# Performance work log

Hardware: AMD Instinct MI355X
Metric: run time of the kernel (lower is better)

## Reference

```python
import jax, jax.numpy as jnp
import numpy as np

D_MODEL = 1024
N_HEADS = 16
D_FF = 4 * D_MODEL
EPS = 1e-5


def _layer_norm(x, g, b):
    mu = jnp.mean(x, axis=-1, keepdims=True)
    var = jnp.mean(jnp.square(x - mu), axis=-1, keepdims=True)
    return (x - mu) * jax.lax.rsqrt(var + EPS) * g + b


def _mha(x, Wq, Wk, Wv, Wo, causal):
    B, S, D = x.shape
    H = N_HEADS
    Dh = D // H
    q = (x @ Wq).reshape(B, S, H, Dh)
    k = (x @ Wk).reshape(B, S, H, Dh)
    v = (x @ Wv).reshape(B, S, H, Dh)
    scores = jnp.einsum('bqhd,bkhd->bhqk', q, k) / jnp.sqrt(jnp.asarray(Dh, x.dtype))
    if causal:
        mask = jnp.tril(jnp.ones((S, S), dtype=bool))  # [S,S] causal mask
        scores = jnp.where(mask, scores, jnp.asarray(-1e9, x.dtype))
    attn = jax.nn.softmax(scores, axis=-1)
    out = jnp.einsum('bhqk,bkhd->bqhd', attn, v).reshape(B, S, D)
    return out @ Wo


def _ffn(x, W1, b1, W2, b2):
    return jax.nn.relu(x @ W1 + b1) @ W2 + b2


def setup_inputs() -> dict:
    key = jax.random.key(0)
    ks = jax.random.split(key, 12)
    sd = 1.0 / np.sqrt(D_MODEL)
    sf = 1.0 / np.sqrt(D_FF)
    B, S = 4, 1024
    return {
        'X': jax.random.normal(ks[0], (B, S, D_MODEL), jnp.float32),
        'Wq1': jax.random.normal(ks[1], (D_MODEL, D_MODEL), jnp.float32) * sd,
        'Wk1': jax.random.normal(ks[2], (D_MODEL, D_MODEL), jnp.float32) * sd,
        'Wv1': jax.random.normal(ks[3], (D_MODEL, D_MODEL), jnp.float32) * sd,
        'Wo1': jax.random.normal(ks[4], (D_MODEL, D_MODEL), jnp.float32) * sd,
        'Wq2': jax.random.normal(ks[5], (D_MODEL, D_MODEL), jnp.float32) * sd,
        'Wk2': jax.random.normal(ks[6], (D_MODEL, D_MODEL), jnp.float32) * sd,
        'Wv2': jax.random.normal(ks[7], (D_MODEL, D_MODEL), jnp.float32) * sd,
        'Wo2': jax.random.normal(ks[8], (D_MODEL, D_MODEL), jnp.float32) * sd,
        'ln_g': jnp.ones((D_MODEL,), jnp.float32),
        'ln_b': jnp.zeros((D_MODEL,), jnp.float32),
        'W1': jax.random.normal(ks[9], (D_MODEL, D_FF), jnp.float32) * sd,
        'b1': jnp.zeros((D_FF,), jnp.float32),
        'W2': jax.random.normal(ks[10], (D_FF, D_MODEL), jnp.float32) * sf,
        'b2': jnp.zeros((D_MODEL,), jnp.float32),
    }


def reference(X, Wq1, Wk1, Wv1, Wo1, Wq2, Wk2, Wv2, Wo2, ln_g, ln_b, W1, b1, W2, b2):
    # Faithful to the torch module (including its unusual residual wiring
    # and the single shared LayerNorm used at all three sites).
    masked = _mha(X, Wq1, Wk1, Wv1, Wo1, causal=True)
    norm_masked = X + _layer_norm(masked, ln_g, ln_b)
    attn2 = _mha(norm_masked, Wq2, Wk2, Wv2, Wo2, causal=False)
    norm_attn2 = attn2 + _layer_norm(attn2, ln_g, ln_b)
    ff = _ffn(norm_attn2, W1, b1, W2, b2)
    return norm_attn2 + _layer_norm(ff, ln_g, ln_b)
```

## Files before the change

kernel.cpp:

```cpp
#include <hip/hip_runtime.h>
#include <hip/hip_bf16.h>

#define D_MODEL 1024
#define N_HEADS 16
#define DH 64
#define D_FF   4096
#define SEQ    1024
#define BATCH  4
#define TOK    (BATCH*SEQ)
#define EPS    1e-5f
#define SCALE  0.125f
#define QSCL   0.18033688f

typedef unsigned short USHORT;
typedef __attribute__((ext_vector_type(8))) short short8v;
typedef __attribute__((ext_vector_type(4))) float f32x4;

__device__ __forceinline__ USHORT f2bf(float f) {
    unsigned int u; __builtin_memcpy(&u, &f, 4);
    u += 0x7fffu + ((u >> 16) & 1u);
    return (USHORT)(u >> 16);
}
__device__ __forceinline__ USHORT f2bf_fast(float f) {
    unsigned int u; __builtin_memcpy(&u, &f, 4);
    return (USHORT)((u + 0x8000u) >> 16);
}
__device__ __forceinline__ unsigned pk2bf(float lo, float hi) {
    __hip_bfloat162 h = __float22bfloat162_rn(make_float2(lo, hi));
    unsigned u; __builtin_memcpy(&u, &h, 4);
    return u;
}
__device__ __forceinline__ float bf2f(USHORT s) {
    unsigned int u = ((unsigned int)s) << 16;
    float f; __builtin_memcpy(&f, &u, 4);
    return f;
}
__device__ __forceinline__ float max3f(float a, float b, float c) {
    return fmaxf(fmaxf(a, b), c);
}

__device__ __forceinline__ short8v ld_frag(const USHORT* lds, int row, int c8) {
    return *reinterpret_cast<const short8v*>(
        &lds[row * 64 + (((c8) ^ (row & 7)) << 3)]);
}
__device__ __forceinline__ short8v ld128(const USHORT* lds, int row, int cu) {
    return *reinterpret_cast<const short8v*>(
        &lds[row * 128 + (((cu) ^ (row & 15)) << 3)]);
}

#define GLDS(gsrc, ldst) \
    __builtin_amdgcn_global_load_lds( \
        (const __attribute__((address_space(1))) void*)(gsrc), \
        (__attribute__((address_space(3))) void*)(ldst), 16, 0, 0)

#define WAITVM(n) asm volatile("s_waitcnt vmcnt(" #n ")" ::: "memory")

__global__ __launch_bounds__(512) void gemm_k256_kernel(
    const USHORT* __restrict__ A, const USHORT* __restrict__ Bt,
    float* __restrict__ Cf, USHORT* __restrict__ Cb, USHORT* __restrict__ Ck,
    USHORT* __restrict__ VtOut,
    int M, int N, int K, const float* __restrict__ bias, int relu, int qkv)
{
    __shared__ USHORT As[2][256 * 64];
    __shared__ USHORT Bs[2][256 * 64];

    const int tid = threadIdx.x;
    const int l   = tid & 63;
    const int w   = tid >> 6;
    const int wr  = w >> 2, wc = w & 3;
    const int lr  = l & 15, lg = l >> 4;

    const int gx  = gridDim.x;
    const int nwg = gx * gridDim.y;
    const int lin = blockIdx.y * gx + blockIdx.x;
    const int swz = (lin & 7) * (nwg >> 3) + (lin >> 3);
    const int m0  = (swz / gx) * 256, n0 = (swz % gx) * 256;

    const USHORT* aS[4]; const USHORT* bS[4]; int dOf[4];
#pragma unroll
    for (int p = 0; p < 4; ++p) {
        const int q = p * 512 + tid;
        const int row = q >> 3, cu = q & 7;
        const int cs = ((cu ^ (row & 7)) << 3);
        aS[p] = A  + (size_t)(m0 + row) * K + cs;
        bS[p] = Bt + (size_t)(n0 + row) * K + cs;
        dOf[p] = (p * 512 + w * 64) * 8;
    }

    auto stage = [&](int buf, int k0) {
#pragma unroll
        for (int p = 0; p < 4; ++p) {
            GLDS(aS[p] + k0, &As[buf][dOf[p]]);
            GLDS(bS[p] + k0, &Bs[buf][dOf[p]]);
        }
    };

    f32x4 acc[8][4];
#pragma unroll
    for (int i = 0; i < 8; ++i)
#pragma unroll
        for (int j = 0; j < 4; ++j) acc[i][j] = (f32x4){0.f, 0.f, 0.f, 0.f};

    const int nk = K >> 6;
    stage(0, 0);

    for (int t = 0; t < nk; ++t) {
        const int cur = t & 1;
        if (t + 1 < nk) {
            stage(cur ^ 1, (t + 1) << 6);
            WAITVM(8);
        } else {
            WAITVM(0);
        }
        __builtin_amdgcn_s_barrier();

#pragma unroll
        for (int ks = 0; ks < 2; ++ks) {
            short8v bfr[4];
#pragma unroll
            for (int ni = 0; ni < 4; ++ni)
                bfr[ni] = ld_frag(Bs[cur], wc * 64 + ni * 16 + lr, ks * 4 + lg);
            __builtin_amdgcn_s_setprio(1);
#pragma unroll
            for (int mi = 0; mi < 8; ++mi) {
                short8v af = ld_frag(As[cur], wr * 128 + mi * 16 + lr, ks * 4 + lg);
#pragma unroll
                for (int ni = 0; ni < 4; ++ni)
                    acc[mi][ni] = __builtin_amdgcn_mfma_f32_16x16x32_bf16(
                        af, bfr[ni], acc[mi][ni], 0, 0, 0);
            }
            __builtin_amdgcn_s_setprio(0);
        }
        __builtin_amdgcn_s_barrier();
    }

    if (qkv) {
#pragma unroll
        for (int mi = 0; mi < 8; ++mi) {
            const int row = m0 + wr * 128 + mi * 16 + (l >> 4) * 4;
#pragma unroll
            for (int ni = 0; ni < 4; ++ni) {
                const int col = n0 + wc * 64 + ni * 16 + lr;
                if (col < 2048) {
                    USHORT* dst = (col < 1024) ? Cb : Ck;
                    const float scl = (col < 1024) ? QSCL : 1.f;
                    const int c = col & 1023;
#pragma unroll
                    for (int j = 0; j < 4; ++j)
                        dst[(size_t)(row + j) * D_MODEL + c] =
                            f2bf(acc[mi][ni][j] * scl);
                } else {
                    const int c = col - 2048;
                    const int bb = row >> 10, jr = row & 1023;
                    const int hh = c >> 6, dd = c & 63;
                    uint2 pk = make_uint2(
                        pk2bf(acc[mi][ni][0], acc[mi][ni][1]),
                        pk2bf(acc[mi][ni][2], acc[mi][ni][3]));
                    *reinterpret_cast<uint2*>(
                        &VtOut[((size_t)(bb * 16 + hh) * 64 + dd) * 1024 + jr]) = pk;
                }
            }
        }
    } else {
#pragma unroll
        for (int mi = 0; mi < 8; ++mi) {
            const int row = m0 + wr * 128 + mi * 16 + (l >> 4) * 4;
#pragma unroll
            for (int ni = 0; ni < 4; ++ni) {
                const int col = n0 + wc * 64 + ni * 16 + lr;
                const float bv = bias ? bias[col] : 0.f;
#pragma unroll
                for (int j = 0; j < 4; ++j) {
                    float v = acc[mi][ni][j] + bv;
                    if (relu) v = fmaxf(v, 0.f);
                    const size_t idx = (size_t)(row + j) * N + col;
                    if (Cf) Cf[idx] = v;
                    if (Cb) Cb[idx] = f2bf(v);
                }
            }
        }
    }
}

__global__ __launch_bounds__(512) void gemm_k128c_kernel(
    const USHORT* __restrict__ A, const USHORT* __restrict__ Bt,
    USHORT* __restrict__ Pa, USHORT* __restrict__ Pb,
    int M, int N, int K)
{
    __shared__ USHORT As[2][128 * 64];
    __shared__ USHORT Bs[2][128 * 64];

    const int tid = threadIdx.x;
    const int l   = tid & 63;
    const int w   = tid >> 6;
    const int wr  = w >> 2, wc = w & 3;
    const int lr  = l & 15, lg = l >> 4;

    const int gx  = gridDim.x;
    const int nwg = gx * gridDim.y;
    const int lin = blockIdx.y * gx + blockIdx.x;
    const int swz = (lin & 7) * (nwg >> 3) + (lin >> 3);
    const int my  = swz / gx;
    const int mt  = M >> 7;
    const int part = my / mt;
    const int m0  = (my % mt) << 7;
    const int n0  = (swz % gx) * 128;
    const int koff = part * (K >> 1);
    USHORT* dst = part ? Pb : Pa;

    const USHORT* aS[2]; const USHORT* bS[2]; int dOf[2];
#pragma unroll
    for (int p = 0; p < 2; ++p) {
        const int q = p * 512 + tid;
        const int row = q >> 3, cu = q & 7;
        const int cs = ((cu ^ (row & 7)) << 3);
        aS[p] = A  + (size_t)(m0 + row) * K + cs;
        bS[p] = Bt + (size_t)(n0 + row) * K + cs;
        dOf[p] = (p * 512 + w * 64) * 8;
    }

    auto stage = [&](int buf, int k0) {
#pragma unroll
        for (int p = 0; p < 2; ++p) {
            GLDS(aS[p] + k0, &As[buf][dOf[p]]);
            GLDS(bS[p] + k0, &Bs[buf][dOf[p]]);
        }
    };

    f32x4 acc[4][2];
#pragma unroll
    for (int i = 0; i < 4; ++i)
#pragma unroll
        for (int j = 0; j < 2; ++j) acc[i][j] = (f32x4){0.f, 0.f, 0.f, 0.f};

    const int nk = K >> 7;
    stage(0, koff);

    for (int t = 0; t < nk; ++t) {
        const int cur = t & 1;
        if (t + 1 < nk) {
            stage(cur ^ 1, koff + ((t + 1) << 6));
            WAITVM(4);
        } else {
            WAITVM(0);
        }
        __builtin_amdgcn_s_barrier();

#pragma unroll
        for (int ks = 0; ks < 2; ++ks) {
            short8v bfr[2];
#pragma unroll
            for (int ni = 0; ni < 2; ++ni)
                bfr[ni] = ld_frag(Bs[cur], wc * 32 + ni * 16 + lr, ks * 4 + lg);
            __builtin_amdgcn_s_setprio(1);
#pragma unroll
            for (int mi = 0; mi < 4; ++mi) {
                short8v af = ld_frag(As[cur], wr * 64 + mi * 16 + lr, ks * 4 + lg);
#pragma unroll
                for (int ni = 0; ni < 2; ++ni)
                    acc[mi][ni] = __builtin_amdgcn_mfma_f32_16x16x32_bf16(
                        af, bfr[ni], acc[mi][ni], 0, 0, 0);
            }
            __builtin_amdgcn_s_setprio(0);
        }
        __builtin_amdgcn_s_barrier();
    }

#pragma unroll
    for (int mi = 0; mi < 4; ++mi) {
        const int row = m0 + wr * 64 + mi * 16 + (l >> 4) * 4;
#pragma unroll
        for (int ni = 0; ni < 2; ++ni) {
            const int col = n0 + wc * 32 + ni * 16 + lr;
#pragma unroll
            for (int j = 0; j < 4; ++j)
                dst[(size_t)(row + j) * N + col] = f2bf(acc[mi][ni][j]);
        }
    }
}

struct TcvtB4 {
    const float* s0; const float* s1; const float* s2; const float* s3;
    USHORT* d0; USHORT* d1; USHORT* d2; USHORT* d3;
};

__device__ __forceinline__ void tcvt_body(
    const float* __restrict__ W, USHORT* __restrict__ Wt, int K, int N)
{
    __shared__ USHORT L[64][65];
    const int tid = threadIdx.x;
    const int tx = tid & 15, ty = tid >> 4;
    const int n0 = blockIdx.x * 64, k0 = blockIdx.y * 64;
#pragma unroll
    for (int r = 0; r < 4; ++r) {
        int kr = ty + 16 * r;
        float4 v = *reinterpret_cast<const float4*>(
            &W[(size_t)(k0 + kr) * N + n0 + tx * 4]);
        L[tx * 4 + 0][kr] = f2bf(v.x);
        L[tx * 4 + 1][kr] = f2bf(v.y);
        L[tx * 4 + 2][kr] = f2bf(v.z);
        L[tx * 4 + 3][kr] = f2bf(v.w);
    }
    __syncthreads();
#pragma unroll
    for (int r = 0; r < 4; ++r) {
        int nr = ty + 16 * r;
        ushort4 o = make_ushort4(L[nr][tx * 4 + 0], L[nr][tx * 4 + 1],
                                 L[nr][tx * 4 + 2], L[nr][tx * 4 + 3]);
        *reinterpret_cast<ushort4*>(&Wt[(size_t)(n0 + nr) * K + k0 + tx * 4]) = o;
    }
}

__global__ __launch_bounds__(256) void tcvt_kernel(
    const float* __restrict__ W, USHORT* __restrict__ Wt, int K, int N)
{
    tcvt_body(W, Wt, K, N);
}

__global__ __launch_bounds__(256) void tcvt4_kernel(TcvtB4 p, int K, int N)
{
    const int z = blockIdx.z;
    const float* W = (z == 0) ? p.s0 : (z == 1) ? p.s1 : (z == 2) ? p.s2 : p.s3;
    USHORT*    Wt = (z == 0) ? p.d0 : (z == 1) ? p.d1 : (z == 2) ? p.d2 : p.d3;
    tcvt_body(W, Wt, K, N);
}

__global__ __launch_bounds__(256) void f2b_kernel(
    const float* __restrict__ in, USHORT* __restrict__ out, int n4)
{
    int i = blockIdx.x * 256 + threadIdx.x;
    if (i < n4) {
        float4 v = reinterpret_cast<const float4*>(in)[i];
        reinterpret_cast<ushort4*>(out)[i] =
            make_ushort4(f2bf(v.x), f2bf(v.y), f2bf(v.z), f2bf(v.w));
    }
}

__global__ __launch_bounds__(256) void attn_mfma_kernel(
    const USHORT* __restrict__ Q, const USHORT* __restrict__ K,
    const USHORT* __restrict__ Vt, USHORT* __restrict__ O, int causal)
{
    __shared__ USHORT smem[40960];

    const int tid = threadIdx.x;
    const int l  = tid & 63;
    const int w  = tid >> 6;
    const int lr = l & 15;
    const int lg = l >> 4;

    const int lin = blockIdx.y * 16 + blockIdx.x;
    const int swz = (lin & 7) * 128 + (lin >> 3);
    const int qt = swz & 15;
    const int bh = swz >> 4;
    const int h = bh & 15, b = bh >> 4;
    const int q0 = qt * 64;

    const USHORT* gq  = Q  + (size_t)(b * SEQ + q0) * D_MODEL + h * DH;
    const USHORT* gk0 = K  + (size_t)b * SEQ * D_MODEL + h * DH;
    const USHORT* gv0 = Vt + (size_t)bh * DH * SEQ;

    auto stageK = [&](int buf, int kt) {
        USHORT* dst = smem + buf * 8192;
        const size_t base = (size_t)kt * 128 * 1024;
#pragma unroll
        for (int p = 0; p < 4; ++p) {
            const int q = p * 256 + tid;
            const int row = q >> 3, cu = q & 7;
            GLDS(gk0 + base + (size_t)row * 1024 + ((cu ^ (row & 7)) << 3),
                 dst + (p * 256 + w * 64) * 8);
        }
    };
    auto stageV = [&](int buf, int kt) {
        USHORT* dst = smem + 16384 + buf * 8192;
        const int j0 = kt * 128;
#pragma unroll
        for (int p = 0; p < 4; ++p) {
            const int q = p * 256 + tid;
            const int row = q >> 4, cu = q & 15;
            GLDS(gv0 + (size_t)row * 1024 + j0 + ((cu ^ (row & 15)) << 3),
                 dst + (p * 256 + w * 64) * 8);
        }
    };

#pragma unroll
    for (int p = 0; p < 2; ++p) {
        const int q = p * 256 + tid;
        const int row = q >> 3, cu = q & 7;
        GLDS(gq + (size_t)row * 1024 + ((cu ^ (row & 7)) << 3),
             smem + 32768 + (p * 256 + w * 64) * 8);
    }
    stageK(0, 0);
    stageV(0, 0);

    f32x4 oacc[4];
    float m_ = -1e30f, l_ = 0.f;
#pragma unroll
    for (int d = 0; d < 4; ++d) oacc[d] = (f32x4){0.f, 0.f, 0.f, 0.f};

    int paddr[8];
#pragma unroll
    for (int jb = 0; jb < 8; ++jb) {
        const int cu = jb * 2 + (lg >> 1);
        paddr[jb] = lr * 128 + ((cu ^ lr) << 3) + (lg & 1) * 4;
    }

    __syncthreads();
    short8v qa0 = ld_frag(smem + 32768, w * 16 + lr, lg);
    short8v qa1 = ld_frag(smem + 32768, w * 16 + lr, 4 + lg);
    __syncthreads();
    USHORT* PsW = smem + 32768 + w * 2048;

    const int ntile = causal ? (qt >> 1) + 1 : (SEQ / 128);
    for (int kt = 0; kt < ntile; ++kt) {
        const int cur = kt & 1;
        if (kt + 1 < ntile) {
            stageK(cur ^ 1, kt + 1);
            stageV(cur ^ 1, kt + 1);
        }
        const int j0 = kt * 128;
        const USHORT* KsC = smem + cur * 8192;
        const USHORT* VsC = smem + 16384 + cur * 8192;

        f32x4 sa[8];
        __builtin_amdgcn_s_setprio(1);
#pragma unroll
        for (int jb = 0; jb < 8; ++jb) {
            sa[jb] = (f32x4){0.f, 0.f, 0.f, 0.f};
            sa[jb] = __builtin_amdgcn_mfma_f32_16x16x32_bf16(
                ld_frag(KsC, jb * 16 + lr, lg), qa0, sa[jb], 0, 0, 0);
            sa[jb] = __builtin_amdgcn_mfma_f32_16x16x32_bf16(
                ld_frag(KsC, jb * 16 + lr, 4 + lg), qa1, sa[jb], 0, 0, 0);
        }
        __builtin_amdgcn_s_setprio(0);

        if (causal && kt == ntile - 1) {
#pragma unroll
            for (int jb = 0; jb < 8; ++jb)
#pragma unroll
                for (int r = 0; r < 4; ++r)
                    if ((j0 + jb * 16 + lg * 4 + r) > (q0 + w * 16 + lr))
                        sa[jb][r] = -1e30f;
        }

        float tm = max3f(
            max3f(max3f(sa[0][0], sa[0][1], sa[0][2]),
                  max3f(sa[0][3], sa[1][0], sa[1][1]),
                  max3f(sa[1][2], sa[1][3], sa[2][0])),
            max3f(max3f(sa[2][1], sa[2][2], sa[2][3]),
                  max3f(sa[3][0], sa[3][1], sa[3][2]),
                  max3f(sa[3][3], sa[4][0], sa[4][1])),
            max3f(max3f(max3f(sa[4][2], sa[4][3], sa[5][0]),
                        max3f(sa[5][1], sa[5][2], sa[5][3]),
                        max3f(sa[6][0], sa[6][1], sa[6][2])),
                  max3f(sa[6][3], sa[7][0], sa[7][1]),
                  fmaxf(sa[7][2], sa[7][3])));
        tm = fmaxf(tm, __shfl_xor(tm, 16));
        tm = fmaxf(tm, __shfl_xor(tm, 32));

        if (__ballot(tm > m_ + 8.f)) {
            const float mn = (tm > m_ + 8.f) ? tm : m_;
            const float sc = exp2f(m_ - mn);
            l_ *= sc;
            m_ = mn;
#pragma unroll
            for (int r = 0; r < 4; ++r) {
                const float scr = __shfl(sc, (l & 48) | (lg * 4 + r));
#pragma unroll
                for (int d = 0; d < 4; ++d) oacc[d][r] *= scr;
            }
        }

#pragma unroll
        for (int jb = 0; jb < 8; ++jb) {
            const float p0 = exp2f(sa[jb][0] - m_);
            const float p1 = exp2f(sa[jb][1] - m_);
            const float p2 = exp2f(sa[jb][2] - m_);
            const float p3 = exp2f(sa[jb][3] - m_);
            l_ += (p0 + p1) + (p2 + p3);
            *reinterpret_cast<uint2*>(&PsW[paddr[jb]]) =
                make_uint2(pk2bf(p0, p1), pk2bf(p2, p3));
        }

        __builtin_amdgcn_s_setprio(1);
#pragma unroll
        for (int ks = 0; ks < 4; ++ks) {
            short8v pa = ld128(PsW, lr, ks * 4 + lg);
#pragma unroll
            for (int d = 0; d < 4; ++d)
                oacc[d] = __builtin_amdgcn_mfma_f32_16x16x32_bf16(
                    pa, ld128(VsC, d * 16 + lr, ks * 4 + lg), oacc[d], 0, 0, 0);
        }
        __builtin_amdgcn_s_setprio(0);
        __syncthreads();
    }

    float lv = l_;
    lv += __shfl_xor(lv, 16);
    lv += __shfl_xor(lv, 32);
    const float inv_own = 1.f / lv;

    USHORT* go = O + (size_t)(b * SEQ + q0 + w * 16) * D_MODEL + h * DH;
#pragma unroll
    for (int r = 0; r < 4; ++r) {
        const float inv = __shfl(inv_own, (l & 48) | (lg * 4 + r));
        const int qrow = lg * 4 + r;
#pragma unroll
        for (int d = 0; d < 4; ++d)
            go[(size_t)qrow * D_MODEL + d * 16 + lr] = f2bf_fast(oacc[d][r] * inv);
    }
}

__global__ __launch_bounds__(256) void ln_res_kernel(
    const USHORT* __restrict__ xb, const USHORT* __restrict__ xb2,
    const float* __restrict__ biasx,
    const float* __restrict__ resf, const USHORT* __restrict__ resb,
    const float* __restrict__ g, const float* __restrict__ bta,
    float* __restrict__ outf, USHORT* __restrict__ outb)
{
    __shared__ float red[256];
    __shared__ float s_mu, s_rstd;

    const int row = blockIdx.x;
    const int tid = threadIdx.x;
    ushort4 xv = reinterpret_cast<const ushort4*>(xb + (size_t)row * D_MODEL)[tid];
    float vx = bf2f(xv.x), vy = bf2f(xv.y), vz = bf2f(xv.z), vw = bf2f(xv.w);
    if (xb2) {
        ushort4 x2 = reinterpret_cast<const ushort4*>(
            xb2 + (size_t)row * D_MODEL)[tid];
        vx += bf2f(x2.x); vy += bf2f(x2.y); vz += bf2f(x2.z); vw += bf2f(x2.w);
    }
    if (biasx) {
        float4 bx = reinterpret_cast<const float4*>(biasx)[tid];
        vx += bx.x; vy += bx.y; vz += bx.z; vw += bx.w;
    }

    red[tid] = vx + vy + vz + vw;
    __syncthreads();
    for (int s = 128; s > 0; s >>= 1) {
        if (tid < s) red[tid] += red[tid + s];
        __syncthreads();
    }
    if (tid == 0) s_mu = red[0] * (1.f / D_MODEL);
    __syncthreads();
    const float mu = s_mu;

    float dx = vx - mu, dy = vy - mu, dz = vz - mu, dw = vw - mu;
    red[tid] = dx * dx + dy * dy + dz * dz + dw * dw;
    __syncthreads();
    for (int s = 128; s > 0; s >>= 1) {
        if (tid < s) red[tid] += red[tid + s];
        __syncthreads();
    }
    if (tid == 0) s_rstd = rsqrtf(red[0] * (1.f / D_MODEL) + EPS);
    __syncthreads();
    const float rstd = s_rstd;

    float4 rv;
    if (resf) {
        rv = reinterpret_cast<const float4*>(resf + (size_t)row * D_MODEL)[tid];
    } else if (resb) {
        ushort4 rb = reinterpret_cast<const ushort4*>(
            resb + (size_t)row * D_MODEL)[tid];
        rv = make_float4(bf2f(rb.x), bf2f(rb.y), bf2f(rb.z), bf2f(rb.w));
    } else {
        rv = make_float4(vx, vy, vz, vw);
    }
    float4 gv = reinterpret_cast<const float4*>(g)[tid];
    float4 bv = reinterpret_cast<const float4*>(bta)[tid];

    float4 o;
    o.x = rv.x + dx * rstd * gv.x + bv.x;
    o.y = rv.y + dy * rstd * gv.y + bv.y;
    o.z = rv.z + dz * rstd * gv.z + bv.z;
    o.w = rv.w + dw * rstd * gv.w + bv.w;
    reinterpret_cast<float4*>(outf + (size_t)row * D_MODEL)[tid] = o;
    if (outb)
        reinterpret_cast<ushort4*>(outb + (size_t)row * D_MODEL)[tid] =
            make_ushort4(f2bf(o.x), f2bf(o.y), f2bf(o.z), f2bf(o.w));
}

extern "C" void kernel_launch(void* const* d_in, const int* in_sizes, int n_in,
                              void* d_out, int out_size, void* d_ws, size_t ws_size,
                              hipStream_t stream)
{
    const float* X    = (const float*)d_in[0];
    const float* Wq1  = (const float*)d_in[1];
    const float* Wk1  = (const float*)d_in[2];
    const float* Wv1  = (const float*)d_in[3];
    const float* Wo1  = (const float*)d_in[4];
    const float* Wq2  = (const float*)d_in[5];
    const float* Wk2  = (const float*)d_in[6];
    const float* Wv2  = (const float*)d_in[7];
    const float* Wo2  = (const float*)d_in[8];
    const float* ln_g = (const float*)d_in[9];
    const float* ln_b = (const float*)d_in[10];
    const float* W1   = (const float*)d_in[11];
    const float* b1   = (const float*)d_in[12];
    const float* W2   = (const float*)d_in[13];
    const float* b2   = (const float*)d_in[14];

    const size_t MI = 1024 * 1024;
    USHORT* ws16 = (USHORT*)d_ws;
    USHORT* Wqkv1t = ws16;
    USHORT* scr0   = ws16;
    USHORT* Wo1t   = ws16 + 3 * MI;
    USHORT* Wqkv2t = ws16 + 4 * MI;
    USHORT* Wo2t   = ws16 + 7 * MI;
    USHORT* W2t    = ws16 + 8 * MI;
    USHORT* Xb     = ws16 + 12 * MI;
    USHORT* W1t    = Xb;
    USHORT* qb     = ws16 + 16 * MI;
    USHORT* kb     = ws16 + 20 * MI;
    USHORT* Vtb    = ws16 + 24 * MI;
    USHORT* t0b    = ws16 + 28 * MI;
    USHORT* hb     = qb;
    USHORT* t2b    = ws16 + 32 * MI;
    USHORT* t1b    = ws16 + 36 * MI;
    float*  t2     = (float*)(ws16 + 40 * MI);

    auto gemm256 = [&](const USHORT* A, const USHORT* Bt, float* Cf, USHORT* Cb,
                       int M, int N, int K, const float* bias, int relu) {
        gemm_k256_kernel<<<dim3(N / 256, M / 256), 512, 0, stream>>>(
            A, Bt, Cf, Cb, nullptr, nullptr, M, N, K, bias, relu, 0);
    };
    auto gemm_qkv = [&](const USHORT* A, const USHORT* Bt) {
        gemm_k256_kernel<<<dim3(3072 / 256, TOK / 256), 512, 0, stream>>>(
            A, Bt, nullptr, qb, kb, Vtb, TOK, 3072, D_MODEL, nullptr, 0, 1);
    };
    auto gemm128c = [&](const USHORT* A, const USHORT* Bt, USHORT* Pa, USHORT* Pb,
                        int M, int N, int K) {
        gemm_k128c_kernel<<<dim3(N / 128, (M / 128) * 2), 512, 0, stream>>>(
            A, Bt, Pa, Pb, M, N, K);
    };

    dim3 agrid(SEQ / 64, BATCH * N_HEADS);

    {
        TcvtB4 p1{Wq1, Wk1, Wv1, Wo1,
                  Wqkv1t, Wqkv1t + 1 * MI, Wqkv1t + 2 * MI, Wo1t};
        tcvt4_kernel<<<dim3(16, 16, 4), 256, 0, stream>>>(p1, D_MODEL, D_MODEL);
        TcvtB4 p2{Wq2, Wk2, Wv2, Wo2,
                  Wqkv2t, Wqkv2t + 1 * MI, Wqkv2t + 2 * MI, Wo2t};
        tcvt4_kernel<<<dim3(16, 16, 4), 256, 0, stream>>>(p2, D_MODEL, D_MODEL);
    }
    tcvt_kernel<<<dim3(D_MODEL / 64, D_FF / 64), 256, 0, stream>>>(
        W2, W2t, D_FF, D_MODEL);
    f2b_kernel<<<dim3(4096), 256, 0, stream>>>(X, Xb, TOK * D_MODEL / 4);

    gemm_qkv(Xb, Wqkv1t);
    attn_mfma_kernel<<<agrid, 256, 0, stream>>>(qb, kb, Vtb, t0b, 1);
    gemm128c(t0b, Wo1t, t2b, t1b, TOK, D_MODEL, D_MODEL);
    ln_res_kernel<<<dim3(TOK), 256, 0, stream>>>(t2b, t1b, nullptr, X, nullptr,
                                                 ln_g, ln_b, t2, t2b);
    tcvt_kernel<<<dim3(D_FF / 64, D_MODEL / 64), 256, 0, stream>>>(
        W1, W1t, D_MODEL, D_FF);

    gemm_qkv(t2b, Wqkv2t);
    attn_mfma_kernel<<<agrid, 256, 0, stream>>>(qb, kb, Vtb, t0b, 0);
    gemm128c(t0b, Wo2t, scr0, t1b, TOK, D_MODEL, D_MODEL);
    ln_res_kernel<<<dim3(TOK), 256, 0, stream>>>(scr0, t1b, nullptr,
                                                 nullptr, nullptr,
                                                 ln_g, ln_b, t2, t2b);

    gemm256(t2b, W1t, nullptr, hb, TOK, D_FF, D_MODEL, b1, 1);
    gemm128c(hb, W2t, t2b, t1b, TOK, D_MODEL, D_FF);
    ln_res_kernel<<<dim3(TOK), 256, 0, stream>>>(t2b, t1b, b2, t2, nullptr,
                                                 ln_g, ln_b, (float*)d_out, nullptr);
}
```

Measured before the change: 338.3 us.

## Retile attention to 128-query blocks with 64-key tiles, two subtiles per wave

The attention kernel now processes 128 query rows per block, with each wave owning two 16-row subtiles, and streams K/V in 64-key tiles instead of 128. Each K and V fragment loaded from LDS is reused across two MFMA subtiles, and shared memory per block shrinks. The intent is to halve K/V global and LDS traffic per query and improve MFMA density. In exchange the grid is halved, which may reduce occupancy and load balance (especially for causal), and more registers are used per thread.

```diff
diff --git a/kernel.cpp b/kernel.cpp
--- a/kernel.cpp
+++ b/kernel.cpp
@@ -42,10 +42,6 @@
 __device__ __forceinline__ short8v ld_frag(const USHORT* lds, int row, int c8) {
     return *reinterpret_cast<const short8v*>(
         &lds[row * 64 + (((c8) ^ (row & 7)) << 3)]);
-}
-__device__ __forceinline__ short8v ld128(const USHORT* lds, int row, int cu) {
-    return *reinterpret_cast<const short8v*>(
-        &lds[row * 128 + (((cu) ^ (row & 15)) << 3)]);
 }
 
 #define GLDS(gsrc, ldst) \
@@ -340,7 +336,7 @@
     const USHORT* __restrict__ Q, const USHORT* __restrict__ K,
     const USHORT* __restrict__ Vt, USHORT* __restrict__ O, int causal)
 {
-    __shared__ USHORT smem[40960];
+    __shared__ USHORT smem[24576];
 
     const int tid = threadIdx.x;
     const int l  = tid & 63;
@@ -348,22 +344,22 @@
     const int lr = l & 15;
     const int lg = l >> 4;
 
-    const int lin = blockIdx.y * 16 + blockIdx.x;
-    const int swz = (lin & 7) * 128 + (lin >> 3);
-    const int qt = swz & 15;
-    const int bh = swz >> 4;
+    const int lin = blockIdx.y * 8 + blockIdx.x;
+    const int swz = (lin & 7) * 64 + (lin >> 3);
+    const int qt = swz & 7;
+    const int bh = swz >> 3;
     const int h = bh & 15, b = bh >> 4;
-    const int q0 = qt * 64;
+    const int q0 = qt * 128;
 
     const USHORT* gq  = Q  + (size_t)(b * SEQ + q0) * D_MODEL + h * DH;
     const USHORT* gk0 = K  + (size_t)b * SEQ * D_MODEL + h * DH;
     const USHORT* gv0 = Vt + (size_t)bh * DH * SEQ;
 
     auto stageK = [&](int buf, int kt) {
-        USHORT* dst = smem + buf * 8192;
-        const size_t base = (size_t)kt * 128 * 1024;
-#pragma unroll
-        for (int p = 0; p < 4; ++p) {
+        USHORT* dst = smem + buf * 4096;
+        const size_t base = (size_t)kt * 64 * 1024;
+#pragma unroll
+        for (int p = 0; p < 2; ++p) {
             const int q = p * 256 + tid;
             const int row = q >> 3, cu = q & 7;
             GLDS(gk0 + base + (size_t)row * 1024 + ((cu ^ (row & 7)) << 3),
@@ -371,142 +367,181 @@
         }
     };
     auto stageV = [&](int buf, int kt) {
-        USHORT* dst = smem + 16384 + buf * 8192;
-        const int j0 = kt * 128;
-#pragma unroll
-        for (int p = 0; p < 4; ++p) {
+        USHORT* dst = smem + 8192 + buf * 4096;
+        const int j0 = kt * 64;
+#pragma unroll
+        for (int p = 0; p < 2; ++p) {
             const int q = p * 256 + tid;
-            const int row = q >> 4, cu = q & 15;
-            GLDS(gv0 + (size_t)row * 1024 + j0 + ((cu ^ (row & 15)) << 3),
+            const int row = q >> 3, cu = q & 7;
+            GLDS(gv0 + (size_t)row * 1024 + j0 + ((cu ^ (row & 7)) << 3),
                  dst + (p * 256 + w * 64) * 8);
         }
     };
 
 #pragma unroll
-    for (int p = 0; p < 2; ++p) {
+    for (int p = 0; p < 4; ++p) {
         const int q = p * 256 + tid;
         const int row = q >> 3, cu = q & 7;
         GLDS(gq + (size_t)row * 1024 + ((cu ^ (row & 7)) << 3),
-             smem + 32768 + (p * 256 + w * 64) * 8);
+             smem + 16384 + (p * 256 + w * 64) * 8);
     }
     stageK(0, 0);
     stageV(0, 0);
 
-    f32x4 oacc[4];
-    float m_ = -1e30f, l_ = 0.f;
-#pragma unroll
-    for (int d = 0; d < 4; ++d) oacc[d] = (f32x4){0.f, 0.f, 0.f, 0.f};
-
-    int paddr[8];
-#pragma unroll
-    for (int jb = 0; jb < 8; ++jb) {
-        const int cu = jb * 2 + (lg >> 1);
-        paddr[jb] = lr * 128 + ((cu ^ lr) << 3) + (lg & 1) * 4;
+    f32x4 oacc[2][4];
+    float m_[2], l_[2];
+#pragma unroll
+    for (int s = 0; s < 2; ++s) {
+        m_[s] = -1e30f; l_[s] = 0.f;
+#pragma unroll
+        for (int d = 0; d < 4; ++d) oacc[s][d] = (f32x4){0.f, 0.f, 0.f, 0.f};
+    }
+
+    int paddr[2][4];
+#pragma unroll
+    for (int s = 0; s < 2; ++s) {
+        const int row = s * 16 + lr;
+#pragma unroll
+        for (int jb = 0; jb < 4; ++jb) {
+            const int cu = jb * 2 + (lg >> 1);
+            paddr[s][jb] = row * 64 + ((cu ^ (row & 7)) << 3) + (lg & 1) * 4;
+        }
     }
 
     __syncthreads();
-    short8v qa0 = ld_frag(smem + 32768, w * 16 + lr, lg);
-    short8v qa1 = ld_frag(smem + 32768, w * 16 + lr, 4 + lg);
+    short8v qa[2][2];
+#pragma unroll
+    for (int s = 0; s < 2; ++s) {
+        qa[s][0] = ld_frag(smem + 16384, w * 32 + s * 16 + lr, lg);
+        qa[s][1] = ld_frag(smem + 16384, w * 32 + s * 16 + lr, 4 + lg);
+    }
     __syncthreads();
-    USHORT* PsW = smem + 32768 + w * 2048;
-
-    const int ntile = causal ? (qt >> 1) + 1 : (SEQ / 128);
+    USHORT* PsW = smem + 16384 + w * 2048;
+
+    const int ntile = causal ? (qt * 2 + 2) : (SEQ / 64);
     for (int kt = 0; kt < ntile; ++kt) {
         const int cur = kt & 1;
         if (kt + 1 < ntile) {
             stageK(cur ^ 1, kt + 1);
             stageV(cur ^ 1, kt + 1);
         }
-        const int j0 = kt * 128;
-        const USHORT* KsC = smem + cur * 8192;
-        const USHORT* VsC = smem + 16384 + cur * 8192;
-
-        f32x4 sa[8];
+        const int j0 = kt * 64;
+        const USHORT* KsC = smem + cur * 4096;
+        const USHORT* VsC = smem + 8192 + cur * 4096;
+
+        f32x4 sa[2][4];
         __builtin_amdgcn_s_setprio(1);
 #pragma unroll
-        for (int jb = 0; jb < 8; ++jb) {
-            sa[jb] = (f32x4){0.f, 0.f, 0.f, 0.f};
-            sa[jb] = __builtin_amdgcn_mfma_f32_16x16x32_bf16(
-                ld_frag(KsC, jb * 16 + lr, lg), qa0, sa[jb], 0, 0, 0);
-            sa[jb] = __builtin_amdgcn_mfma_f32_16x16x32_bf16(
-                ld_frag(KsC, jb * 16 + lr, 4 + lg), qa1, sa[jb], 0, 0, 0);
+        for (int jb = 0; jb < 4; ++jb) {
+            short8v kf0 = ld_frag(KsC, jb * 16 + lr, lg);
+            short8v kf1 = ld_frag(KsC, jb * 16 + lr, 4 + lg);
+#pragma unroll
+            for (int s = 0; s < 2; ++s) {
+                sa[s][jb] = (f32x4){0.f, 0.f, 0.f, 0.f};
+                sa[s][jb] = __builtin_amdgcn_mfma_f32_16x16x32_bf16(
+                    kf0, qa[s][0], sa[s][jb], 0, 0, 0);
+                sa[s][jb] = __builtin_amdgcn_mfma_f32_16x16x32_bf16(
+                    kf1, qa[s][1], sa[s][jb], 0, 0, 0);
+            }
         }
         __builtin_amdgcn_s_setprio(0);
 
-        if (causal && kt == ntile - 1) {
-#pragma unroll
-            for (int jb = 0; jb < 8; ++jb)
-#pragma unroll
-                for (int r = 0; r < 4; ++r)
-                    if ((j0 + jb * 16 + lg * 4 + r) > (q0 + w * 16 + lr))
-                        sa[jb][r] = -1e30f;
-        }
-
-        float tm = max3f(
-            max3f(max3f(sa[0][0], sa[0][1], sa[0][2]),
-                  max3f(sa[0][3], sa[1][0], sa[1][1]),
-                  max3f(sa[1][2], sa[1][3], sa[2][0])),
-            max3f(max3f(sa[2][1], sa[2][2], sa[2][3]),
-                  max3f(sa[3][0], sa[3][1], sa[3][2]),
-                  max3f(sa[3][3], sa[4][0], sa[4][1])),
-            max3f(max3f(max3f(sa[4][2], sa[4][3], sa[5][0]),
-                        max3f(sa[5][1], sa[5][2], sa[5][3]),
-                        max3f(sa[6][0], sa[6][1], sa[6][2])),
-                  max3f(sa[6][3], sa[7][0], sa[7][1]),
-                  fmaxf(sa[7][2], sa[7][3])));
-        tm = fmaxf(tm, __shfl_xor(tm, 16));
-        tm = fmaxf(tm, __shfl_xor(tm, 32));
-
-        if (__ballot(tm > m_ + 8.f)) {
-            const float mn = (tm > m_ + 8.f) ? tm : m_;
-            const float sc = exp2f(m_ - mn);
-            l_ *= sc;
-            m_ = mn;
-#pragma unroll
-            for (int r = 0; r < 4; ++r) {
-                const float scr = __shfl(sc, (l & 48) | (lg * 4 + r));
-#pragma unroll
-                for (int d = 0; d < 4; ++d) oacc[d][r] *= scr;
-            }
-        }
-
-#pragma unroll
-        for (int jb = 0; jb < 8; ++jb) {
-            const float p0 = exp2f(sa[jb][0] - m_);
-            const float p1 = exp2f(sa[jb][1] - m_);
-            const float p2 = exp2f(sa[jb][2] - m_);
-            const float p3 = exp2f(sa[jb][3] - m_);
-            l_ += (p0 + p1) + (p2 + p3);
-            *reinterpret_cast<uint2*>(&PsW[paddr[jb]]) =
-                make_uint2(pk2bf(p0, p1), pk2bf(p2, p3));
-        }
+        if (causal && kt >= ntile - 2) {
+#pragma unroll
+            for (int s = 0; s < 2; ++s) {
+                const int qrow = q0 + w * 32 + s * 16 + lr;
+#pragma unroll
+                for (int jb = 0; jb < 4; ++jb)
+#pragma unroll
+                    for (int r = 0; r < 4; ++r)
+                        if ((j0 + jb * 16 + lg * 4 + r) > qrow)
+                            sa[s][jb][r] = -1e30f;
+            }
+        }
+
+        float tm[2];
+#pragma unroll
+        for (int s = 0; s < 2; ++s) {
+            float t1 = max3f(sa[s][0][0], sa[s][0][1], sa[s][0][2]);
+            float t2 = max3f(sa[s][0][3], sa[s][1][0], sa[s][1][1]);
+            float t3 = max3f(sa[s][1][2], sa[s][1][3], sa[s][2][0]);
+            float t4 = max3f(sa[s][2][1], sa[s][2][2], sa[s][2][3]);
+            float t5 = max3f(sa[s][3][0], sa[s][3][1], sa[s][3][2]);
+            float tv = fmaxf(max3f(max3f(t1, t2, t3), t4, t5), sa[s][3][3]);
+            tv = fmaxf(tv, __shfl_xor(tv, 16));
+            tv = fmaxf(tv, __shfl_xor(tv, 32));
+            tm[s] = tv;
+        }
+
+        const bool anyf = (tm[0] > m_[0] + 8.f) | (tm[1] > m_[1] + 8.f);
+        if (__ballot(anyf)) {
+            float sc[2];
+#pragma unroll
+            for (int s = 0; s < 2; ++s) {
+                const float mn = (tm[s] > m_[s] + 8.f) ? tm[s] : m_[s];
+                sc[s] = exp2f(m_[s] - mn);
+                l_[s] *= sc[s];
+                m_[s] = mn;
+            }
+#pragma unroll
+            for (int s = 0; s < 2; ++s)
+#pragma unroll
+                for (int r = 0; r < 4; ++r) {
+                    const float scr = __shfl(sc[s], (l & 48) | (lg * 4 + r));
+#pragma unroll
+                    for (int d = 0; d < 4; ++d) oacc[s][d][r] *= scr;
+                }
+        }
+
+#pragma unroll
+        for (int s = 0; s < 2; ++s)
+#pragma unroll
+            for (int jb = 0; jb < 4; ++jb) {
+                const float p0 = exp2f(sa[s][jb][0] - m_[s]);
+                const float p1 = exp2f(sa[s][jb][1] - m_[s]);
+                const float p2 = exp2f(sa[s][jb][2] - m_[s]);
+                const float p3 = exp2f(sa[s][jb][3] - m_[s]);
+                l_[s] += (p0 + p1) + (p2 + p3);
+                *reinterpret_cast<uint2*>(&PsW[paddr[s][jb]]) =
+                    make_uint2(pk2bf(p0, p1), pk2bf(p2, p3));
+            }
 
         __builtin_amdgcn_s_setprio(1);
 #pragma unroll
-        for (int ks = 0; ks < 4; ++ks) {
-            short8v pa = ld128(PsW, lr, ks * 4 + lg);
-#pragma unroll
-            for (int d = 0; d < 4; ++d)
-                oacc[d] = __builtin_amdgcn_mfma_f32_16x16x32_bf16(
-                    pa, ld128(VsC, d * 16 + lr, ks * 4 + lg), oacc[d], 0, 0, 0);
+        for (int ks = 0; ks < 2; ++ks) {
+            short8v pa[2];
+#pragma unroll
+            for (int s = 0; s < 2; ++s)
+                pa[s] = ld_frag(PsW, s * 16 + lr, ks * 4 + lg);
+#pragma unroll
+            for (int d = 0; d < 4; ++d) {
+                short8v vf = ld_frag(VsC, d * 16 + lr, ks * 4 + lg);
+#pragma unroll
+                for (int s = 0; s < 2; ++s)
+                    oacc[s][d] = __builtin_amdgcn_mfma_f32_16x16x32_bf16(
+                        pa[s], vf, oacc[s][d], 0, 0, 0);
+            }
         }
         __builtin_amdgcn_s_setprio(0);
         __syncthreads();
     }
 
-    float lv = l_;
-    lv += __shfl_xor(lv, 16);
-    lv += __shfl_xor(lv, 32);
-    const float inv_own = 1.f / lv;
-
-    USHORT* go = O + (size_t)(b * SEQ + q0 + w * 16) * D_MODEL + h * DH;
-#pragma unroll
-    for (int r = 0; r < 4; ++r) {
-        const float inv = __shfl(inv_own, (l & 48) | (lg * 4 + r));
-        const int qrow = lg * 4 + r;
-#pragma unroll
-        for (int d = 0; d < 4; ++d)
-            go[(size_t)qrow * D_MODEL + d * 16 + lr] = f2bf_fast(oacc[d][r] * inv);
+    USHORT* go = O + (size_t)(b * SEQ + q0 + w * 32) * D_MODEL + h * DH;
+#pragma unroll
+    for (int s = 0; s < 2; ++s) {
+        float lv = l_[s];
+        lv += __shfl_xor(lv, 16);
+        lv += __shfl_xor(lv, 32);
+        const float inv_own = 1.f / lv;
+#pragma unroll
+        for (int r = 0; r < 4; ++r) {
+            const float inv = __shfl(inv_own, (l & 48) | (lg * 4 + r));
+            const int qrow = s * 16 + lg * 4 + r;
+#pragma unroll
+            for (int d = 0; d < 4; ++d)
+                go[(size_t)qrow * D_MODEL + d * 16 + lr] =
+                    f2bf_fast(oacc[s][d][r] * inv);
+        }
     }
 }
 
@@ -633,7 +668,7 @@
             A, Bt, Pa, Pb, M, N, K);
     };
 
-    dim3 agrid(SEQ / 64, BATCH * N_HEADS);
+    dim3 agrid(SEQ / 128, BATCH * N_HEADS);
 
     {
         TcvtB4 p1{Wq1, Wk1, Wv1, Wo1,
```

Measured after the change: 335.1 us. About the same (-1.0%).
